# Kernel tuning notes

Measured on AMD Instinct MI355X. Metric: run time of the kernel, lower is better.

The kernel has to match this reference:

```python
import jax, jax.numpy as jnp
import numpy as np

B, D, H, O, E = 16384, 1024, 512, 256, 8


def setup_inputs() -> dict:
    key = jax.random.key(0)
    ks = jax.random.split(key, 8)
    s = lambda k, shape, fan: (jax.random.normal(k, shape, jnp.float32) / np.sqrt(fan).astype(np.float32))
    z = lambda shape: jnp.zeros(shape, jnp.float32)
    return {
        "x": jax.random.normal(ks[0], (B, D), jnp.float32),
        # gating network: D -> 256 -> 128 -> E
        "gw1": s(ks[1], (D, 256), D), "gb1": z((256,)),
        "gw2": s(ks[2], (256, 128), 256), "gb2": z((128,)),
        "gw3": s(ks[3], (128, E), 128), "gb3": z((E,)),
        # experts, batched over expert dim E: D -> H -> H -> O
        "ew1": s(ks[4], (E, D, H), D), "eb1": z((E, H)),
        "ew2": s(ks[5], (E, H, H), H), "eb2": z((E, H)),
        "ew3": s(ks[6], (E, H, O), H), "eb3": z((E, O)),
    }


def reference(x, gw1, gb1, gw2, gb2, gw3, gb3, ew1, eb1, ew2, eb2, ew3, eb3):
    # Gating network (dropout is identity in eval mode)
    g = jax.nn.relu(x @ gw1 + gb1)
    g = jax.nn.relu(g @ gw2 + gb2)
    gates = jax.nn.softmax(g @ gw3 + gb3, axis=1)  # [B, E]
    # All experts run on every token: batched small MLPs over expert axis e
    h = jax.nn.relu(jnp.einsum('bd,edh->ebh', x, ew1) + eb1[:, None, :])   # [E, B, H]
    h = jax.nn.relu(jnp.einsum('ebh,ehk->ebk', h, ew2) + eb2[:, None, :])  # [E, B, H]
    eo = jnp.einsum('ebh,eho->ebo', h, ew3) + eb3[:, None, :]              # [E, B, O]
    # gate-weighted sum over experts
    out = jnp.einsum('ebo,be->bo', eo, gates)  # [B, O]
    return out
```

## Files before the change

### kernel.cpp

```cpp
#include <hip/hip_runtime.h>
#include <hip/hip_bf16.h>

typedef __hip_bfloat16 bf16;
typedef __attribute__((ext_vector_type(8))) __bf16 bf16x8;
typedef __attribute__((ext_vector_type(4))) float f32x4;

#define B_ 16384
#define D_ 1024
#define H_ 512
#define O_ 256
#define E_ 8
#define BC_ 8192

#define GLDS(src, dst) __builtin_amdgcn_global_load_lds( \
    (const __attribute__((address_space(1))) void*)(src), \
    (__attribute__((address_space(3))) void*)(dst), 16, 0, 0)

__global__ void detect_k(const unsigned short* __restrict__ x, int* __restrict__ flag) {
    __shared__ int s;
    if (threadIdx.x == 0) s = 0;
    __syncthreads();
    int big = 0;
    for (int i = threadIdx.x; i < 2048; i += 256)
        if (((x[i] >> 7) & 0xFF) >= 150) big = 1;
    if (big) atomicOr(&s, 1);
    __syncthreads();
    if (threadIdx.x == 0) *flag = s;
}

__global__ void cvt_k(const void* __restrict__ src, bf16* __restrict__ dst,
                      const int* __restrict__ flag, long n) {
    const int f = *flag;
    long i = (long)blockIdx.x * blockDim.x + threadIdx.x;
    const long stride = (long)gridDim.x * blockDim.x;
    if (f) {
        const float* s = (const float*)src;
        for (; i < n; i += stride) dst[i] = __float2bfloat16(s[i]);
    } else {
        const bf16* s = (const bf16*)src;
        for (; i < n; i += stride) dst[i] = s[i];
    }
}

__global__ void transpose_k(const void* __restrict__ in, bf16* __restrict__ out,
                            const int* __restrict__ flag, int R, int C) {
    __shared__ bf16 t[32][33];
    const int f = *flag;
    const long zo = (long)blockIdx.z * R * C;
    const int x = blockIdx.x * 32 + threadIdx.x;
    const int y0 = blockIdx.y * 32;
    const float* inf = (const float*)in;
    const bf16* inb = (const bf16*)in;
#pragma unroll
    for (int i = 0; i < 4; i++) {
        int r = y0 + threadIdx.y + i * 8;
        long idx = zo + (long)r * C + x;
        t[threadIdx.y + i * 8][threadIdx.x] =
            f ? __float2bfloat16(inf[idx]) : inb[idx];
    }
    __syncthreads();
    const int xr = blockIdx.y * 32 + threadIdx.x;
#pragma unroll
    for (int i = 0; i < 4; i++) {
        int c = blockIdx.x * 32 + threadIdx.y + i * 8;
        out[zo + (long)c * R + xr] = t[threadIdx.x][threadIdx.y + i * 8];
    }
}

__global__ void gate3_softmax_k(const bf16* __restrict__ g2,
                                const bf16* __restrict__ gw3,
                                const bf16* __restrict__ gb3,
                                float* __restrict__ gates) {
    __shared__ float w[128 * 8];
    __shared__ float bsh[8];
    const int tid = threadIdx.x;
    for (int i = tid; i < 1024; i += 256) w[i] = __bfloat162float(gw3[i]);
    if (tid < 8) bsh[tid] = __bfloat162float(gb3[tid]);
    __syncthreads();

    const long row = (long)blockIdx.x * 256 + tid;
    float acc[8];
#pragma unroll
    for (int o = 0; o < 8; o++) acc[o] = bsh[o];

    const bf16x8* rp8 = (const bf16x8*)(g2 + row * 128);
#pragma unroll 4
    for (int c8 = 0; c8 < 16; c8++) {
        bf16x8 v8 = rp8[c8];
#pragma unroll
        for (int jj = 0; jj < 8; jj++) {
            float v = (float)v8[jj];
            int k = c8 * 8 + jj;
#pragma unroll
            for (int o = 0; o < 8; o++) acc[o] += v * w[k * 8 + o];
        }
    }
    float m = acc[0];
#pragma unroll
    for (int o = 1; o < 8; o++) m = fmaxf(m, acc[o]);
    float s = 0.f;
#pragma unroll
    for (int o = 0; o < 8; o++) { acc[o] = __expf(acc[o] - m); s += acc[o]; }
    const float inv = 1.f / s;
#pragma unroll
    for (int o = 0; o < 8; o++) gates[row * 8 + o] = acc[o] * inv;
}

template <int MODE>
__global__ __launch_bounds__(256, 4)
void gemm_bt(const bf16* __restrict__ A, const bf16* __restrict__ Bt,
             const bf16* __restrict__ bias, const float* __restrict__ gates,
             void* __restrict__ Cout, const bf16* __restrict__ eb3,
             const int* __restrict__ oflag,
             int lda, int ldb, int ldo, int K,
             long a_z, long b_z, long bias_z, long out_z,
             int e_gate, int k_per_e, long a_e, long b_e, long row0) {
    __shared__ __attribute__((aligned(16))) bf16 As[128 * 32];
    __shared__ __attribute__((aligned(16))) bf16 Bs[128 * 32];

    const int tid  = threadIdx.x;
    const int lane = tid & 63;
    const int quad = lane >> 4;
    const int l15  = lane & 15;
    const int wid  = tid >> 6;
    const int wr   = (wid >> 1) << 6;
    const int wc   = (wid & 1) << 6;
    const int z    = blockIdx.z;
    const long m0  = (long)blockIdx.y << 7;
    const long n0  = (long)blockIdx.x << 7;

    const bf16* Az = A + (long)z * a_z;
    const bf16* Bz = Bt + (long)z * b_z;

    f32x4 acc[4][4];
#pragma unroll
    for (int i = 0; i < 4; i++)
#pragma unroll
        for (int j = 0; j < 4; j++) acc[i][j] = (f32x4){0.f, 0.f, 0.f, 0.f};

    const int erow = tid >> 2;
    const int ecol = (tid & 3) << 3;

    const int n_e   = k_per_e ? (K / k_per_e) : 1;
    const int inner = (k_per_e ? k_per_e : K) >> 5;

    for (int e = 0; e < n_e; e++) {
        const bf16* Ae = Az + (long)e * a_e;
        const bf16* Be = Bz + (long)e * b_e;
        for (int kti = 0; kti < inner; kti++) {
            const int kk = kti << 5;
#pragma unroll
            for (int i = 0; i < 2; i++) {
                const int r = (i << 6) + erow;
                GLDS(Ae + (m0 + r) * lda + (kk + ecol), As + r * 32 + ecol);
            }
#pragma unroll
            for (int i = 0; i < 2; i++) {
                const int r = (i << 6) + erow;
                GLDS(Be + (n0 + r) * ldb + (kk + ecol), Bs + r * 32 + ecol);
            }
            __syncthreads();
            bf16x8 af[4], bfr[4];
#pragma unroll
            for (int i = 0; i < 4; i++)
                af[i] = *(const bf16x8*)(As + (wr + i * 16 + l15) * 32 + (quad << 3));
#pragma unroll
            for (int j = 0; j < 4; j++)
                bfr[j] = *(const bf16x8*)(Bs + (wc + j * 16 + l15) * 32 + (quad << 3));
#pragma unroll
            for (int i = 0; i < 4; i++)
#pragma unroll
                for (int j = 0; j < 4; j++)
                    acc[i][j] = __builtin_amdgcn_mfma_f32_16x16x32_bf16(
                        af[i], bfr[j], acc[i][j], 0, 0, 0);
            __syncthreads();
        }
    }

    const int eg = (e_gate >= 0) ? e_gate : z;

    if constexpr (MODE == 0 || MODE == 1) {
        bf16* C = (bf16*)Cout + (long)z * out_z;
        const bf16* bb = bias + (long)z * bias_z;
        float gv[4][4];
        if constexpr (MODE == 1) {
#pragma unroll
            for (int i = 0; i < 4; i++)
#pragma unroll
                for (int rg = 0; rg < 4; rg++)
                    gv[i][rg] = gates[(row0 + m0 + wr + i * 16 + quad * 4 + rg) * 8 + eg];
        }
#pragma unroll
        for (int j = 0; j < 4; j++) {
            const int c = (int)n0 + wc + j * 16 + l15;
            const float bv = __bfloat162float(bb[c]);
#pragma unroll
            for (int i = 0; i < 4; i++) {
#pragma unroll
                for (int rg = 0; rg < 4; rg++) {
                    const long r = m0 + wr + i * 16 + quad * 4 + rg;
                    float v = fmaxf(acc[i][j][rg] + bv, 0.f);
                    if constexpr (MODE == 1) v *= gv[i][rg];
                    C[r * ldo + c] = __float2bfloat16(v);
                }
            }
        }
    } else if constexpr (MODE == 2) {
        float* C = (float*)Cout;
#pragma unroll
        for (int i = 0; i < 4; i++) {
#pragma unroll
            for (int rg = 0; rg < 4; rg++) {
                const long r = m0 + wr + i * 16 + quad * 4 + rg;
                const float g = gates[(row0 + r) * 8 + eg];
#pragma unroll
                for (int j = 0; j < 4; j++) {
                    const int c = (int)n0 + wc + j * 16 + l15;
                    const float b3 = __bfloat162float(eb3[eg * O_ + c]);
                    C[r * ldo + c] += acc[i][j][rg] + g * b3;
                }
            }
        }
    } else {
        float* C = (float*)Cout + (long)z * out_z;
        const int e0 = z * 2;
        float b30[4], b31[4];
#pragma unroll
        for (int j = 0; j < 4; j++) {
            const int c = (int)n0 + wc + j * 16 + l15;
            b30[j] = __bfloat162float(eb3[e0 * O_ + c]);
            b31[j] = __bfloat162float(eb3[(e0 + 1) * O_ + c]);
        }
#pragma unroll
        for (int i = 0; i < 4; i++) {
#pragma unroll
            for (int rg = 0; rg < 4; rg++) {
                const long r = m0 + wr + i * 16 + quad * 4 + rg;
                const float g0 = gates[(row0 + r) * 8 + e0];
                const float g1 = gates[(row0 + r) * 8 + e0 + 1];
#pragma unroll
                for (int j = 0; j < 4; j++) {
                    const int c = (int)n0 + wc + j * 16 + l15;
                    C[(row0 + r) * ldo + c] =
                        acc[i][j][rg] + g0 * b30[j] + g1 * b31[j];
                }
            }
        }
    }
}

__global__ void zero_f32_k(float* __restrict__ p) {
    p[(long)blockIdx.x * 256 + threadIdx.x] = 0.f;
}
__global__ void out_cvt_k(const float* __restrict__ in, void* __restrict__ out,
                          const int* __restrict__ flag) {
    const long i = (long)blockIdx.x * 256 + threadIdx.x;
    if (*flag) ((float*)out)[i] = in[i];
    else       ((bf16*)out)[i] = __float2bfloat16(in[i]);
}
__global__ void reduce4_k(const float* __restrict__ p, void* __restrict__ out,
                          const int* __restrict__ flag) {
    const long n = (long)B_ * O_;
    const long i = ((long)blockIdx.x * 256 + threadIdx.x) * 4;
    float4 a = *(const float4*)(p + i);
    float4 b = *(const float4*)(p + n + i);
    float4 c = *(const float4*)(p + 2 * n + i);
    float4 d = *(const float4*)(p + 3 * n + i);
    float4 s = {a.x + b.x + c.x + d.x, a.y + b.y + c.y + d.y,
                a.z + b.z + c.z + d.z, a.w + b.w + c.w + d.w};
    if (*flag) {
        *(float4*)((float*)out + i) = s;
    } else {
        bf16* o = (bf16*)out + i;
        o[0] = __float2bfloat16(s.x); o[1] = __float2bfloat16(s.y);
        o[2] = __float2bfloat16(s.z); o[3] = __float2bfloat16(s.w);
    }
}

extern "C" void kernel_launch(void* const* d_in, const int* in_sizes, int n_in,
                              void* d_out, int out_size, void* d_ws, size_t ws_size,
                              hipStream_t stream) {
    (void)in_sizes; (void)n_in; (void)out_size;
    const void* x   = d_in[0];
    const void* gw1 = d_in[1];
    const void* gb1 = d_in[2];
    const void* gw2 = d_in[3];
    const void* gb2 = d_in[4];
    const void* gw3 = d_in[5];
    const void* gb3 = d_in[6];
    const void* ew1 = d_in[7];
    const void* eb1 = d_in[8];
    const void* ew2 = d_in[9];
    const void* eb2 = d_in[10];
    const void* ew3 = d_in[11];
    const void* eb3 = d_in[12];

    char* ws = (char*)d_ws;
    size_t off = 0;
    auto alloc = [&](size_t n) { char* p = ws + off; off += (n + 255) & ~(size_t)255; return p; };

    int*  flag  = (int*)alloc(256);
    bf16* xc    = (bf16*)alloc((size_t)B_ * D_ * 2);
    bf16* gw1t  = (bf16*)alloc((size_t)256 * 1024 * 2);
    bf16* gw2t  = (bf16*)alloc((size_t)128 * 256 * 2);
    bf16* ew1t  = (bf16*)alloc((size_t)E_ * H_ * D_ * 2);
    bf16* ew2t  = (bf16*)alloc((size_t)E_ * H_ * H_ * 2);
    bf16* ew3t  = (bf16*)alloc((size_t)E_ * O_ * H_ * 2);
    bf16* gb1c  = (bf16*)alloc(256 * 2);
    bf16* gb2c  = (bf16*)alloc(128 * 2);
    bf16* gw3c  = (bf16*)alloc(1024 * 2);
    bf16* gb3c  = (bf16*)alloc(8 * 2);
    bf16* eb1c  = (bf16*)alloc((size_t)E_ * H_ * 2);
    bf16* eb2c  = (bf16*)alloc((size_t)E_ * H_ * 2);
    bf16* eb3c  = (bf16*)alloc((size_t)E_ * O_ * 2);
    bf16* g1    = (bf16*)alloc((size_t)B_ * 256 * 2);
    bf16* g2b   = (bf16*)alloc((size_t)B_ * 128 * 2);
    float* gates = (float*)alloc((size_t)B_ * 8 * 4);

    const size_t small = off;
    const size_t needA = small + 2ull * ((size_t)E_ * BC_ * H_ * 2 + 256)
                               + (4ull * B_ * O_ * 4 + 256) + 4096;
    const bool pathA = ws_size >= needA;

    detect_k<<<1, 256, 0, stream>>>((const unsigned short*)x, flag);

    cvt_k<<<4096, 256, 0, stream>>>(x, xc, flag, (long)B_ * D_);
    cvt_k<<<1, 256, 0, stream>>>(gb1, gb1c, flag, 256);
    cvt_k<<<1, 256, 0, stream>>>(gb2, gb2c, flag, 128);
    cvt_k<<<4, 256, 0, stream>>>(gw3, gw3c, flag, 1024);
    cvt_k<<<1, 256, 0, stream>>>(gb3, gb3c, flag, 8);
    cvt_k<<<16, 256, 0, stream>>>(eb1, eb1c, flag, (long)E_ * H_);
    cvt_k<<<16, 256, 0, stream>>>(eb2, eb2c, flag, (long)E_ * H_);
    cvt_k<<<8, 256, 0, stream>>>(eb3, eb3c, flag, (long)E_ * O_);

    transpose_k<<<dim3(256 / 32, 1024 / 32, 1), dim3(32, 8), 0, stream>>>(gw1, gw1t, flag, 1024, 256);
    transpose_k<<<dim3(128 / 32, 256 / 32, 1), dim3(32, 8), 0, stream>>>(gw2, gw2t, flag, 256, 128);
    transpose_k<<<dim3(H_ / 32, D_ / 32, E_), dim3(32, 8), 0, stream>>>(ew1, ew1t, flag, D_, H_);
    transpose_k<<<dim3(H_ / 32, H_ / 32, E_), dim3(32, 8), 0, stream>>>(ew2, ew2t, flag, H_, H_);
    transpose_k<<<dim3(O_ / 32, H_ / 32, E_), dim3(32, 8), 0, stream>>>(ew3, ew3t, flag, H_, O_);

    gemm_bt<0><<<dim3(2, 128, 1), 256, 0, stream>>>(
        xc, gw1t, gb1c, nullptr, g1, nullptr, nullptr,
        1024, 1024, 256, 1024, 0, 0, 0, 0, 0, 0, 0, 0, 0);
    gemm_bt<0><<<dim3(1, 128, 1), 256, 0, stream>>>(
        g1, gw2t, gb2c, nullptr, g2b, nullptr, nullptr,
        256, 256, 128, 256, 0, 0, 0, 0, 0, 0, 0, 0, 0);
    gate3_softmax_k<<<dim3(B_ / 256), 256, 0, stream>>>(g2b, gw3c, gb3c, gates);

    if (pathA) {
        bf16* h1c = (bf16*)alloc((size_t)E_ * BC_ * H_ * 2);
        bf16* h2c = (bf16*)alloc((size_t)E_ * BC_ * H_ * 2);
        float* parts = (float*)alloc(4ull * B_ * O_ * 4);
        for (int ci = 0; ci < B_ / BC_; ci++) {
            const long rb = (long)ci * BC_;
            gemm_bt<0><<<dim3(4, BC_ / 128, 8), 256, 0, stream>>>(
                xc + rb * D_, ew1t, eb1c, nullptr, h1c, nullptr, nullptr,
                D_, D_, H_, D_,
                0, (long)H_ * D_, H_, (long)BC_ * H_, 0, 0, 0, 0, 0);
            gemm_bt<1><<<dim3(4, BC_ / 128, 8), 256, 0, stream>>>(
                h1c, ew2t, eb2c, gates, h2c, nullptr, nullptr,
                H_, H_, H_, H_,
                (long)BC_ * H_, (long)H_ * H_, H_, (long)BC_ * H_, -1, 0, 0, 0, rb);
            gemm_bt<5><<<dim3(2, BC_ / 128, 4), 256, 0, stream>>>(
                h2c, ew3t, nullptr, gates, parts, eb3c, nullptr,
                H_, H_, O_, 1024,
                2L * BC_ * H_, 2L * O_ * H_, 0, (long)B_ * O_,
                2 , 512, (long)BC_ * H_, (long)O_ * H_, rb);
        }
        reduce4_k<<<dim3(B_ * O_ / 1024), 256, 0, stream>>>(parts, d_out, flag);
    } else {
        bf16* h1s = (bf16*)alloc((size_t)B_ * H_ * 2);
        bf16* h2s = (bf16*)alloc((size_t)B_ * H_ * 2);
        float* oacc = (float*)alloc((size_t)B_ * O_ * 4);
        zero_f32_k<<<dim3(B_ * O_ / 256), 256, 0, stream>>>(oacc);
        for (int e = 0; e < E_; e++) {
            gemm_bt<0><<<dim3(4, 128, 1), 256, 0, stream>>>(
                xc, ew1t + (size_t)e * H_ * D_, eb1c + (size_t)e * H_, nullptr, h1s, nullptr, nullptr,
                1024, 1024, 512, 1024, 0, 0, 0, 0, 0, 0, 0, 0, 0);
            gemm_bt<1><<<dim3(4, 128, 1), 256, 0, stream>>>(
                h1s, ew2t + (size_t)e * H_ * H_, eb2c + (size_t)e * H_, gates, h2s, nullptr, nullptr,
                512, 512, 512, 512, 0, 0, 0, 0, e, 0, 0, 0, 0);
            gemm_bt<2><<<dim3(2, 128, 1), 256, 0, stream>>>(
                h2s, ew3t + (size_t)e * O_ * H_, nullptr, gates, oacc, eb3c, nullptr,
                512, 512, 256, 512, 0, 0, 0, 0, e, 0, 0, 0, 0);
        }
        out_cvt_k<<<dim3(B_ * O_ / 256), 256, 0, stream>>>(oacc, d_out, flag);
    }
}
```

Before: 591.2 us.

## Swizzle GEMM LDS tiles, merge small conversions, split-K gating GEMMs

Changes the global-to-LDS load mapping so each thread writes contiguous LDS slots with a rotated column order, and reads fragments with a matching XOR-like offset to avoid LDS bank conflicts. Merges seven tiny conversion launches into one single-block kernel to cut launch overhead. On path A, the two gating GEMMs become split-K over two z-slices with fp32 partials, plus a combine kernel that adds bias and applies ReLU. This raises parallelism for the small gating GEMMs at the cost of extra fp32 traffic and two more launches.

After: 603.8 us. 2.1% more time.

```diff
diff --git a/kernel.cpp b/kernel.cpp
--- a/kernel.cpp
+++ b/kernel.cpp
@@ -42,6 +42,21 @@
     }
 }
 
+__global__ void cvt_multi_k(const void* gb1, const void* gb2, const void* gw3,
+                            const void* gb3, const void* eb1, const void* eb2,
+                            const void* eb3,
+                            bf16* gb1c, bf16* gb2c, bf16* gw3c, bf16* gb3c,
+                            bf16* eb1c, bf16* eb2c, bf16* eb3c,
+                            const int* __restrict__ flag) {
+    const int f = *flag;
+    auto cv = [&](const void* s, bf16* d, int n) {
+        for (int i = threadIdx.x; i < n; i += 256)
+            d[i] = f ? __float2bfloat16(((const float*)s)[i]) : ((const bf16*)s)[i];
+    };
+    cv(gb1, gb1c, 256); cv(gb2, gb2c, 128); cv(gw3, gw3c, 1024); cv(gb3, gb3c, 8);
+    cv(eb1, eb1c, E_ * H_); cv(eb2, eb2c, E_ * H_); cv(eb3, eb3c, E_ * O_);
+}
+
 __global__ void transpose_k(const void* __restrict__ in, bf16* __restrict__ out,
                             const int* __restrict__ flag, int R, int C) {
     __shared__ bf16 t[32][33];
@@ -138,8 +153,9 @@
 #pragma unroll
         for (int j = 0; j < 4; j++) acc[i][j] = (f32x4){0.f, 0.f, 0.f, 0.f};
 
-    const int erow = tid >> 2;
-    const int ecol = (tid & 3) << 3;
+    const int srow = tid >> 2;
+    const int scol = (((tid & 3) - (tid >> 3)) & 3) << 3;
+    const int dlt  = (((quad + (l15 >> 1)) & 3) << 3);
 
     const int n_e   = k_per_e ? (K / k_per_e) : 1;
     const int inner = (k_per_e ? k_per_e : K) >> 5;
@@ -149,24 +165,18 @@
         const bf16* Be = Bz + (long)e * b_e;
         for (int kti = 0; kti < inner; kti++) {
             const int kk = kti << 5;
-#pragma unroll
-            for (int i = 0; i < 2; i++) {
-                const int r = (i << 6) + erow;
-                GLDS(Ae + (m0 + r) * lda + (kk + ecol), As + r * 32 + ecol);
-            }
-#pragma unroll
-            for (int i = 0; i < 2; i++) {
-                const int r = (i << 6) + erow;
-                GLDS(Be + (n0 + r) * ldb + (kk + ecol), Bs + r * 32 + ecol);
-            }
+            GLDS(Ae + (m0 + srow) * lda + (kk + scol),       As + (tid << 3));
+            GLDS(Ae + (m0 + 64 + srow) * lda + (kk + scol),  As + ((tid + 256) << 3));
+            GLDS(Be + (n0 + srow) * ldb + (kk + scol),       Bs + (tid << 3));
+            GLDS(Be + (n0 + 64 + srow) * ldb + (kk + scol),  Bs + ((tid + 256) << 3));
             __syncthreads();
             bf16x8 af[4], bfr[4];
 #pragma unroll
             for (int i = 0; i < 4; i++)
-                af[i] = *(const bf16x8*)(As + (wr + i * 16 + l15) * 32 + (quad << 3));
+                af[i] = *(const bf16x8*)(As + (wr + i * 16 + l15) * 32 + dlt);
 #pragma unroll
             for (int j = 0; j < 4; j++)
-                bfr[j] = *(const bf16x8*)(Bs + (wc + j * 16 + l15) * 32 + (quad << 3));
+                bfr[j] = *(const bf16x8*)(Bs + (wc + j * 16 + l15) * 32 + dlt);
 #pragma unroll
             for (int i = 0; i < 4; i++)
 #pragma unroll
@@ -221,7 +231,7 @@
                 }
             }
         }
-    } else {
+    } else if constexpr (MODE == 5) {
         float* C = (float*)Cout + (long)z * out_z;
         const int e0 = z * 2;
         float b30[4], b31[4];
@@ -246,6 +256,20 @@
                 }
             }
         }
+    } else {
+        float* C = (float*)Cout + (long)z * out_z;
+#pragma unroll
+        for (int i = 0; i < 4; i++) {
+#pragma unroll
+            for (int rg = 0; rg < 4; rg++) {
+                const long r = m0 + wr + i * 16 + quad * 4 + rg;
+#pragma unroll
+                for (int j = 0; j < 4; j++) {
+                    const int c = (int)n0 + wc + j * 16 + l15;
+                    C[r * ldo + c] = acc[i][j][rg];
+                }
+            }
+        }
     }
 }
 
@@ -257,6 +281,15 @@
     const long i = (long)blockIdx.x * 256 + threadIdx.x;
     if (*flag) ((float*)out)[i] = in[i];
     else       ((bf16*)out)[i] = __float2bfloat16(in[i]);
+}
+__global__ void combine_relu_k(const float* __restrict__ p,
+                               const bf16* __restrict__ bias,
+                               bf16* __restrict__ out, int ncmask, long n) {
+    const long i = (long)blockIdx.x * 256 + threadIdx.x;
+    if (i < n) {
+        float v = p[i] + p[n + i] + __bfloat162float(bias[i & ncmask]);
+        out[i] = __float2bfloat16(fmaxf(v, 0.f));
+    }
 }
 __global__ void reduce4_k(const float* __restrict__ p, void* __restrict__ out,
                           const int* __restrict__ flag) {
@@ -325,13 +358,9 @@
     detect_k<<<1, 256, 0, stream>>>((const unsigned short*)x, flag);
 
     cvt_k<<<4096, 256, 0, stream>>>(x, xc, flag, (long)B_ * D_);
-    cvt_k<<<1, 256, 0, stream>>>(gb1, gb1c, flag, 256);
-    cvt_k<<<1, 256, 0, stream>>>(gb2, gb2c, flag, 128);
-    cvt_k<<<4, 256, 0, stream>>>(gw3, gw3c, flag, 1024);
-    cvt_k<<<1, 256, 0, stream>>>(gb3, gb3c, flag, 8);
-    cvt_k<<<16, 256, 0, stream>>>(eb1, eb1c, flag, (long)E_ * H_);
-    cvt_k<<<16, 256, 0, stream>>>(eb2, eb2c, flag, (long)E_ * H_);
-    cvt_k<<<8, 256, 0, stream>>>(eb3, eb3c, flag, (long)E_ * O_);
+    cvt_multi_k<<<1, 256, 0, stream>>>(gb1, gb2, gw3, gb3, eb1, eb2, eb3,
+                                       gb1c, gb2c, gw3c, gb3c, eb1c, eb2c, eb3c,
+                                       flag);
 
     transpose_k<<<dim3(256 / 32, 1024 / 32, 1), dim3(32, 8), 0, stream>>>(gw1, gw1t, flag, 1024, 256);
     transpose_k<<<dim3(128 / 32, 256 / 32, 1), dim3(32, 8), 0, stream>>>(gw2, gw2t, flag, 256, 128);
@@ -339,18 +368,27 @@
     transpose_k<<<dim3(H_ / 32, H_ / 32, E_), dim3(32, 8), 0, stream>>>(ew2, ew2t, flag, H_, H_);
     transpose_k<<<dim3(O_ / 32, H_ / 32, E_), dim3(32, 8), 0, stream>>>(ew3, ew3t, flag, H_, O_);
 
-    gemm_bt<0><<<dim3(2, 128, 1), 256, 0, stream>>>(
-        xc, gw1t, gb1c, nullptr, g1, nullptr, nullptr,
-        1024, 1024, 256, 1024, 0, 0, 0, 0, 0, 0, 0, 0, 0);
-    gemm_bt<0><<<dim3(1, 128, 1), 256, 0, stream>>>(
-        g1, gw2t, gb2c, nullptr, g2b, nullptr, nullptr,
-        256, 256, 128, 256, 0, 0, 0, 0, 0, 0, 0, 0, 0);
-    gate3_softmax_k<<<dim3(B_ / 256), 256, 0, stream>>>(g2b, gw3c, gb3c, gates);
-
     if (pathA) {
         bf16* h1c = (bf16*)alloc((size_t)E_ * BC_ * H_ * 2);
         bf16* h2c = (bf16*)alloc((size_t)E_ * BC_ * H_ * 2);
         float* parts = (float*)alloc(4ull * B_ * O_ * 4);
+
+        gemm_bt<6><<<dim3(2, 128, 2), 256, 0, stream>>>(
+            xc, gw1t, nullptr, nullptr, parts, nullptr, nullptr,
+            1024, 1024, 256, 512,
+            512 , 512 , 0, (long)B_ * 256,
+            0, 0, 0, 0, 0);
+        combine_relu_k<<<dim3(B_ * 256 / 256), 256, 0, stream>>>(
+            parts, gb1c, g1, 255, (long)B_ * 256);
+        gemm_bt<6><<<dim3(1, 128, 2), 256, 0, stream>>>(
+            g1, gw2t, nullptr, nullptr, parts, nullptr, nullptr,
+            256, 256, 128, 128,
+            128, 128, 0, (long)B_ * 128,
+            0, 0, 0, 0, 0);
+        combine_relu_k<<<dim3(B_ * 128 / 256), 256, 0, stream>>>(
+            parts, gb2c, g2b, 127, (long)B_ * 128);
+        gate3_softmax_k<<<dim3(B_ / 256), 256, 0, stream>>>(g2b, gw3c, gb3c, gates);
+
         for (int ci = 0; ci < B_ / BC_; ci++) {
             const long rb = (long)ci * BC_;
             gemm_bt<0><<<dim3(4, BC_ / 128, 8), 256, 0, stream>>>(
@@ -369,6 +407,13 @@
         }
         reduce4_k<<<dim3(B_ * O_ / 1024), 256, 0, stream>>>(parts, d_out, flag);
     } else {
+        gemm_bt<0><<<dim3(2, 128, 1), 256, 0, stream>>>(
+            xc, gw1t, gb1c, nullptr, g1, nullptr, nullptr,
+            1024, 1024, 256, 1024, 0, 0, 0, 0, 0, 0, 0, 0, 0);
+        gemm_bt<0><<<dim3(1, 128, 1), 256, 0, stream>>>(
+            g1, gw2t, gb2c, nullptr, g2b, nullptr, nullptr,
+            256, 256, 128, 256, 0, 0, 0, 0, 0, 0, 0, 0, 0);
+        gate3_softmax_k<<<dim3(B_ / 256), 256, 0, stream>>>(g2b, gw3c, gb3c, gates);
         bf16* h1s = (bf16*)alloc((size_t)B_ * H_ * 2);
         bf16* h2s = (bf16*)alloc((size_t)B_ * H_ * 2);
         float* oacc = (float*)alloc((size_t)B_ * O_ * 4);
```
